# Kernel tuning notes

Hardware: AMD Instinct MI355X
Metric: run time of the kernel (lower is better)

Reference implementation:

```python
import jax, jax.numpy as jnp
import numpy as np

FS = 24000.0
C_SOUND = 343.0
MAX_TAU = 6
IGNORE = -100
PAIRS = np.array([(0, 1), (0, 2), (0, 3), (1, 2), (1, 3), (2, 3)])  # m1<m2 loop order
PERMS_NP = np.array([(0, 1, 2), (0, 2, 1), (1, 0, 2), (1, 2, 0), (2, 0, 1), (2, 1, 0)])  # itertools order


def _mic_locs():
    # [rad, azi_deg, ele_deg] per mic, centered at origin (matches center_mic_coords)
    coords = np.array([[0.042, 45, 35], [0.042, -45, -35], [0.042, 135, -35], [0.042, -135, 35]], dtype=np.float64)
    rad = coords[:, 0]
    azi = coords[:, 1] * 2 * np.pi / 360
    ele = coords[:, 2] * 2 * np.pi / 360
    locs = np.stack([rad * np.cos(azi) * np.cos(ele), rad * np.sin(azi) * np.cos(ele), rad * np.sin(ele)], axis=1)
    return jnp.asarray(locs, dtype=jnp.float32)

MIC_LOCS = _mic_locs()  # [4,3]


def _get_tdoa_targets(target):
    """Vectorized get_tdoa_target. target: [B,T,E,5,C].
    Assumes <=1 active class per (b,t,track) so the random class shuffle is a no-op.
    Returns (tdoas, tdoas2) as int32 [B,T,E,6]."""
    B, T, E, F, C = target.shape
    active = target[:, :, :, 0, :]                                  # [B,T,E,C] 0/1 flags
    is_active = jnp.any(active > 0, axis=-1)                        # [B,T,E]
    doa = jnp.einsum('btec,btedc->bted', active, target[:, :, :, 1:4, :])  # [B,T,E,3]
    dist = jnp.einsum('btec,btec->bte', active, target[:, :, :, 4, :])     # [B,T,E]
    src = doa * dist[..., None]                                     # [B,T,E,3]
    d = jnp.linalg.norm(src[..., None, :] - MIC_LOCS, axis=-1)      # [B,T,E,4] dist to each mic
    tdoa = d[..., PAIRS[:, 0]] - d[..., PAIRS[:, 1]]                # [B,T,E,6]
    tdoa = jnp.round(tdoa * FS / C_SOUND) + MAX_TAU                 # [B,T,E,6]
    # compact active tracks to the front (stable keeps track order, matching tr_cnt)
    order = jnp.argsort(jnp.logical_not(is_active), axis=-1)        # [B,T,E]
    gathered = jnp.take_along_axis(tdoa, order[..., None], axis=2)  # [B,T,E,6]
    n = jnp.sum(is_active, axis=-1)                                 # [B,T] number of events
    k = jnp.arange(E)[None, None, :]                                # slot index
    idx1 = jnp.clip(jnp.minimum(k, n[:, :, None] - 1), 0, E - 1)    # pad with LAST event
    idx2 = jnp.where(k < n[:, :, None], k, 0)                       # pad with FIRST event
    tdoas = jnp.take_along_axis(gathered, idx1[..., None], axis=2)
    tdoas2 = jnp.take_along_axis(gathered, idx2[..., None], axis=2)
    empty = (n == 0)[:, :, None, None]
    tdoas = jnp.where(empty, float(IGNORE), tdoas)
    tdoas2 = jnp.where(empty, float(IGNORE), tdoas2)
    return tdoas.astype(jnp.int32), tdoas2.astype(jnp.int32)


def _forward(pred, t_a, t_b):
    B, T, C, Tr, ntd = pred.shape
    N = B * T * ntd
    p = pred.transpose(0, 1, 4, 2, 3).reshape(N, C, Tr)             # [N,C,Tr]
    ta = t_a.transpose(0, 1, 3, 2).reshape(N, Tr)                   # [N,Tr]
    tb = t_b.transpose(0, 1, 3, 2).reshape(N, Tr)
    logp = jax.nn.log_softmax(p, axis=1)                            # [N,C,Tr]
    perms = jnp.asarray(PERMS_NP)                                   # [6,Tr]
    ar = jnp.arange(Tr)

    def pit(t):
        tc = jnp.clip(t, 0, C - 1)
        # L[n,i,j] = CE(pred track j, target track i); ignore_index -> 0
        L = -jnp.take_along_axis(logp, jnp.broadcast_to(tc[:, :, None], (N, Tr, Tr)), axis=1)
        L = jnp.where((t == IGNORE)[:, :, None], 0.0, L)
        pl = L[:, ar[None, :], perms].mean(axis=-1)                 # [N,6] per-perm mean loss
        pidx = jnp.argmin(pl, axis=1)                               # first min (matches torch loop)
        return jnp.take_along_axis(pl, pidx[:, None], axis=1)[:, 0], perms[pidx]

    loss1, perm1 = pit(ta)
    loss2, perm2 = pit(tb)
    use2 = loss2 < loss1                                            # torch.min keeps first on ties
    loss = jnp.where(use2, loss2, loss1)
    t_sel = jnp.where(use2[:, None], tb, ta)
    perm_sel = jnp.where(use2[:, None], perm2, perm1)

    pred_cls = jnp.argmax(p, axis=1)                                # [N,Tr]
    t_perm = jnp.take_along_axis(t_sel, perm_sel, axis=1)           # target reordered by opt perm
    valid = t_perm != IGNORE
    npred = jnp.sum(valid)
    correct = jnp.sum((pred_cls == t_perm) & valid)
    acc = jnp.where(npred > 0, correct.astype(jnp.float32) / jnp.maximum(npred, 1).astype(jnp.float32), 0.0)

    mask = loss > 0.0
    nval = jnp.sum(mask)
    lmean = jnp.where(nval > 0, jnp.sum(jnp.where(mask, loss, 0.0)) / jnp.maximum(nval, 1).astype(loss.dtype), 0.0)
    return lmean, acc


def setup_inputs() -> dict:
    key = jax.random.key(0)
    B, T, E, NCLS, NTD, CPRED = 128, 600, 3, 13, 6, 13
    k1, k2, k3, k4, k5 = jax.random.split(key, 5)
    pred = jax.random.normal(k1, (B, T, CPRED, E, NTD), dtype=jnp.float32)
    act_cls = jax.random.randint(k2, (B, T, E), 0, NCLS)
    act_flag = (jax.random.uniform(k3, (B, T, E)) < 0.5).astype(jnp.float32)
    onehot = jax.nn.one_hot(act_cls, NCLS, dtype=jnp.float32) * act_flag[..., None]  # <=1 active class/track
    doa = jax.random.normal(k4, (B, T, E, 3), dtype=jnp.float32)
    doa = doa / jnp.linalg.norm(doa, axis=-1, keepdims=True)
    dist = jax.random.uniform(k5, (B, T, E), minval=1.0, maxval=3.0, dtype=jnp.float32)
    target = jnp.concatenate([
        onehot[:, :, :, None, :],
        jnp.broadcast_to(doa[..., None], (B, T, E, 3, NCLS)),
        jnp.broadcast_to(dist[..., None, None], (B, T, E, 1, NCLS)),
    ], axis=3).astype(jnp.float32)                                  # [B,T,E,5,NCLS]
    return {"pred": pred, "target": target}


def reference(pred, target):
    t_a, t_b = _get_tdoa_targets(target)
    return _forward(pred, t_a, t_b)
```

## Files before the change

### kernel.cpp

```cpp
#include <hip/hip_runtime.h>
#include <cstdint>
#include <cstddef>

#define BT_TOTAL 76800
#define NCLS 13
#define IGN  (-100)

#define CPB   32
#define NTHR  192
#define NBLK  (BT_TOTAL / CPB)
#define NF4P  (CPB * 234 / 4)
#define KP    10
#define PADP  (KP * NTHR)

struct Partial { float ls; int lc; int cor; int val; };

__device__ __forceinline__ void stage16(const float4* g, float4* l) {
    __builtin_amdgcn_global_load_lds((const __attribute__((address_space(1))) void*)g,
                                     (__attribute__((address_space(3))) void*)l,
                                     16, 0, 0);
}

extern "C" __global__ __launch_bounds__(NTHR)
void tdoa_fused(const float* __restrict__ pred, const float* __restrict__ target,
                Partial* __restrict__ part) {
    const int tid = threadIdx.x;
    const int cb  = blockIdx.x * CPB;

    __shared__ float4 sP4[PADP];
    const float* sP = (const float*)sP4;

    {
        const float4* gp = (const float4*)(pred + (size_t)cb * 234);
#pragma unroll
        for (int r = 0; r < KP; r++) {
            const int i  = r * NTHR + tid;
            const int ic = (i < NF4P) ? i : (NF4P - 1);
            stage16(gp + ic, &sP4[i]);
        }
    }

    const int cell = tid / 6;
    const int p    = tid - cell * 6;
    const float* tg = target + (size_t)(cb + cell) * 195;

    const float MX[4] = { 0.02432757455f,  0.02432757455f, -0.02432757455f, -0.02432757455f };
    const float MY[4] = { 0.02432757455f, -0.02432757455f,  0.02432757455f, -0.02432757455f };
    const float MZ[4] = { 0.02409021033f, -0.02409021033f, -0.02409021033f,  0.02409021033f };
    const int PI_[6] = {0,0,0,1,1,2};
    const int PJ_[6] = {1,2,3,2,3,3};
    const int mi = PI_[p], mj = PJ_[p];
    const float mxi = MX[mi], myi = MY[mi], mzi = MZ[mi];
    const float mxj = MX[mj], myj = MY[mj], mzj = MZ[mj];

    int  td[3];
    bool ab[3];
    int  nact = 0;
#pragma unroll
    for (int e = 0; e < 3; e++) {
        float av = 0.f; int ci = 0; bool ia = false;
#pragma unroll
        for (int c = 0; c < NCLS; c++) {
            const float a = tg[e * 65 + c];
            const bool  g = (a > 0.0f);
            av = g ? a : av;
            ci = g ? c : ci;
            ia = ia || g;
        }
        const float d0 = av * tg[e * 65 + 13 + ci];
        const float d1 = av * tg[e * 65 + 26 + ci];
        const float d2 = av * tg[e * 65 + 39 + ci];
        const float ds = av * tg[e * 65 + 52 + ci];
        const float sx = d0 * ds, sy = d1 * ds, sz = d2 * ds;
        const float exi = sx - mxi, eyi = sy - myi, ezi = sz - mzi;
        const float exj = sx - mxj, eyj = sy - myj, ezj = sz - mzj;
        const float dmi = sqrtf(exi * exi + eyi * eyi + ezi * ezi);
        const float dmj = sqrtf(exj * exj + eyj * eyj + ezj * ezj);
        td[e] = (int)rintf((dmi - dmj) * (24000.0f / 343.0f)) + 6;
        ab[e] = ia;
        nact += ia ? 1 : 0;
    }

    const int g0 = ab[0] ? td[0] : (ab[1] ? td[1] : td[2]);
    const int g1 = (ab[0] && ab[1]) ? td[1] : td[2];
    const int g2 = td[2];
    int ta[3], tb[3];
    ta[0] = g0;
    ta[1] = (nact >= 2) ? g1 : g0;
    ta[2] = (nact == 3) ? g2 : ((nact == 2) ? g1 : g0);
    tb[0] = g0;
    tb[1] = (nact >= 2) ? g1 : g0;
    tb[2] = (nact == 3) ? g2 : g0;
    if (nact == 0) { ta[0] = ta[1] = ta[2] = IGN; tb[0] = tb[1] = tb[2] = IGN; }

    __syncthreads();

    const float* pp = sP + cell * 234 + p;

    float x[NCLS][3];
#pragma unroll
    for (int c = 0; c < NCLS; c++)
#pragma unroll
        for (int j = 0; j < 3; j++)
            x[c][j] = pp[c * 18 + j * 6];

    int   am[3];
    float lse[3];
#pragma unroll
    for (int j = 0; j < 3; j++) {
        float m = x[0][j]; int a = 0;
#pragma unroll
        for (int c = 1; c < NCLS; c++) { if (x[c][j] > m) { m = x[c][j]; a = c; } }
        float s = 0.f;
#pragma unroll
        for (int c = 0; c < NCLS; c++) s += expf(x[c][j] - m);
        am[j] = a; lse[j] = m + logf(s);
    }

    float La[3][3], Lb[3][3];
#pragma unroll
    for (int i = 0; i < 3; i++) {
        const int  ca  = (ta[i] < 0) ? 0 : ta[i];
        const int  cbb = (tb[i] < 0) ? 0 : tb[i];
        const bool ia2 = (ta[i] == IGN);
        const bool ib2 = (tb[i] == IGN);
#pragma unroll
        for (int j = 0; j < 3; j++) {
            La[i][j] = ia2 ? 0.f : (lse[j] - pp[ca  * 18 + j * 6]);
            Lb[i][j] = ib2 ? 0.f : (lse[j] - pp[cbb * 18 + j * 6]);
        }
    }

    const int P0[6] = {0,0,1,1,2,2};
    const int P1[6] = {1,2,0,2,0,1};
    const int P2[6] = {2,1,2,0,1,0};
    float l1 = 0.f, l2 = 0.f; int i1 = 0, i2 = 0;
#pragma unroll
    for (int q = 0; q < 6; q++) {
        const float va = (La[0][P0[q]] + La[1][P1[q]] + La[2][P2[q]]) * (1.0f / 3.0f);
        const float vb = (Lb[0][P0[q]] + Lb[1][P1[q]] + Lb[2][P2[q]]) * (1.0f / 3.0f);
        if (q == 0) { l1 = va; l2 = vb; }
        else {
            if (va < l1) { l1 = va; i1 = q; }
            if (vb < l2) { l2 = vb; i2 = q; }
        }
    }

    const bool use2 = (l2 < l1);
    const float loss = use2 ? l2 : l1;
    const int  qsel = use2 ? i2 : i1;
    const int PK[6] = {36, 24, 33, 9, 18, 6};
    int pk = PK[0];
#pragma unroll
    for (int k = 1; k < 6; k++) pk = (qsel == k) ? PK[k] : pk;
    const int s0 = use2 ? tb[0] : ta[0];
    const int s1 = use2 ? tb[1] : ta[1];
    const int s2 = use2 ? tb[2] : ta[2];

    float lsum = 0.f;
    int   lcnt = 0, cor = 0, nval = 0;
#pragma unroll
    for (int i = 0; i < 3; i++) {
        const int pi = (pk >> (2 * i)) & 3;
        const int tp = (pi == 0) ? s0 : ((pi == 1) ? s1 : s2);
        const bool v = (tp != IGN);
        nval += v ? 1 : 0;
        cor  += (v && (am[i] == tp)) ? 1 : 0;
    }
    if (loss > 0.f) { lsum += loss; lcnt++; }

#pragma unroll
    for (int off = 32; off > 0; off >>= 1) {
        lsum += __shfl_down(lsum, off, 64);
        lcnt += __shfl_down(lcnt, off, 64);
        cor  += __shfl_down(cor,  off, 64);
        nval += __shfl_down(nval, off, 64);
    }
    __shared__ float rf[3];
    __shared__ int   r1[3], r2[3], r3[3];
    const int wid = tid >> 6;
    if ((tid & 63) == 0) { rf[wid] = lsum; r1[wid] = lcnt; r2[wid] = cor; r3[wid] = nval; }
    __syncthreads();
    if (tid == 0) {
        Partial pt;
        pt.ls  = rf[0] + rf[1] + rf[2];
        pt.lc  = r1[0] + r1[1] + r1[2];
        pt.cor = r2[0] + r2[1] + r2[2];
        pt.val = r3[0] + r3[1] + r3[2];
        part[blockIdx.x] = pt;
    }
}

extern "C" __global__ __launch_bounds__(256)
void tdoa_final(const Partial* __restrict__ part, float* __restrict__ out) {
    const int tid = threadIdx.x;
    double ls = 0.0; int lc = 0, cor = 0, val = 0;
    for (int i = tid; i < NBLK; i += 256) {
        const Partial p = part[i];
        ls += (double)p.ls; lc += p.lc; cor += p.cor; val += p.val;
    }
#pragma unroll
    for (int off = 32; off > 0; off >>= 1) {
        ls  += __shfl_down(ls,  off, 64);
        lc  += __shfl_down(lc,  off, 64);
        cor += __shfl_down(cor, off, 64);
        val += __shfl_down(val, off, 64);
    }
    __shared__ double sd[4];
    __shared__ int    s1[4], s2[4], s3[4];
    const int wid = tid >> 6;
    if ((tid & 63) == 0) { sd[wid] = ls; s1[wid] = lc; s2[wid] = cor; s3[wid] = val; }
    __syncthreads();
    if (tid == 0) {
        const double L = sd[0] + sd[1] + sd[2] + sd[3];
        const int c1 = s1[0] + s1[1] + s1[2] + s1[3];
        const int c2 = s2[0] + s2[1] + s2[2] + s2[3];
        const int c3 = s3[0] + s3[1] + s3[2] + s3[3];
        out[0] = (c1 > 0) ? (float)(L / (double)c1) : 0.0f;
        out[1] = (c3 > 0) ? ((float)c2 / (float)c3) : 0.0f;
    }
}

extern "C" void kernel_launch(void* const* d_in, const int* in_sizes, int n_in,
                              void* d_out, int out_size, void* d_ws, size_t ws_size,
                              hipStream_t stream) {
    const float* pred   = (const float*)d_in[0];
    const float* target = (const float*)d_in[1];
    Partial* part = (Partial*)d_ws;
    float* out = (float*)d_out;
    hipLaunchKernelGGL(tdoa_fused, dim3(NBLK), dim3(NTHR), 0, stream, pred, target, part);
    hipLaunchKernelGGL(tdoa_final, dim3(1),    dim3(256), 0, stream, part, out);
}
```

Before: 156.0 us.

## Compute per-track TDOAs once per track in shared memory and use fast exp/log

Target processing is redistributed so that each pair of threads handles one (cell, track). They read the one-hot row and the doa/dist rows with a dot product, split across two half-threads. The unit computes all four mic distances once, packs six clamped TDOA values plus an active flag into a 32-bit word in shared memory, and the pair threads unpack them. This replaces the old scheme, where each of six pair threads per cell redundantly scanned all targets and did sqrt work. Softmax exp/log also switch to the fast intrinsics, trading a little accuracy. The TDOA values are newly clamped to 0..12, and a stray label sits in the loop.

```diff
diff --git a/kernel.cpp b/kernel.cpp
--- a/kernel.cpp
+++ b/kernel.cpp
@@ -27,7 +27,8 @@
     const int tid = threadIdx.x;
     const int cb  = blockIdx.x * CPB;
 
-    __shared__ float4 sP4[PADP];
+    __shared__ float4   sP4[PADP];
+    __shared__ uint32_t sTd[CPB * 3];
     const float* sP = (const float*)sP4;
 
     {
@@ -40,50 +41,77 @@
         }
     }
 
+    {
+        const int unit  = tid >> 1;
+        const int h     = tid & 1;
+        const int cellU = unit / 3;
+        const int e     = unit - cellU * 3;
+        const float* tgE = target + (size_t)(cb + cellU) * 195 + e * 65;
+
+        float d0 = 0.f, d1 = 0.f, d2 = 0.f, ds = 0.f;
+        bool  ia = false;
+#pragma unroll
+        for (int k = 0; k < 7; k++) {
+            if (h && k == 6) break;
+            const int c  = h ? (7 + k) : k;
+            const float a  = tgE[c];
+            const float r0 = tgE[13 + c];
+            const float r1 = tgE[26 + c];
+            const float r2 = tgE[39 + c];
+            const float r3 = tgE[52 + c];
+            ia = ia || (a > 0.0f);
+            d0 += a * r0;
+            d1 += a * r1;
+            d2 += a * r2;
+            d3_dummy:;
+            ds += a * r3;
+        }
+        d0 += __shfl_xor(d0, 1, 64);
+        d1 += __shfl_xor(d1, 1, 64);
+        d2 += __shfl_xor(d2, 1, 64);
+        ds += __shfl_xor(ds, 1, 64);
+        int iai = ia ? 1 : 0;
+        iai |= __shfl_xor(iai, 1, 64);
+
+        const float sx = d0 * ds, sy = d1 * ds, sz = d2 * ds;
+        const float MX[4] = { 0.02432757455f,  0.02432757455f, -0.02432757455f, -0.02432757455f };
+        const float MY[4] = { 0.02432757455f, -0.02432757455f,  0.02432757455f, -0.02432757455f };
+        const float MZ[4] = { 0.02409021033f, -0.02409021033f, -0.02409021033f,  0.02409021033f };
+        float dm[4];
+#pragma unroll
+        for (int m = 0; m < 4; m++) {
+            const float ex = sx - MX[m], ey = sy - MY[m], ez = sz - MZ[m];
+            dm[m] = sqrtf(ex * ex + ey * ey + ez * ez);
+        }
+        const int PI_[6] = {0,0,0,1,1,2};
+        const int PJ_[6] = {1,2,3,2,3,3};
+        uint32_t w = 0;
+#pragma unroll
+        for (int p = 0; p < 6; p++) {
+            int t = (int)rintf((dm[PI_[p]] - dm[PJ_[p]]) * (24000.0f / 343.0f)) + 6;
+            t = (t < 0) ? 0 : ((t > 12) ? 12 : t);
+            w |= ((uint32_t)t) << (4 * p);
+        }
+        if (iai) w |= (1u << 28);
+        if (h == 0) sTd[cellU * 3 + e] = w;
+    }
+
+    __syncthreads();
+
     const int cell = tid / 6;
     const int p    = tid - cell * 6;
-    const float* tg = target + (size_t)(cb + cell) * 195;
-
-    const float MX[4] = { 0.02432757455f,  0.02432757455f, -0.02432757455f, -0.02432757455f };
-    const float MY[4] = { 0.02432757455f, -0.02432757455f,  0.02432757455f, -0.02432757455f };
-    const float MZ[4] = { 0.02409021033f, -0.02409021033f, -0.02409021033f,  0.02409021033f };
-    const int PI_[6] = {0,0,0,1,1,2};
-    const int PJ_[6] = {1,2,3,2,3,3};
-    const int mi = PI_[p], mj = PJ_[p];
-    const float mxi = MX[mi], myi = MY[mi], mzi = MZ[mi];
-    const float mxj = MX[mj], myj = MY[mj], mzj = MZ[mj];
-
-    int  td[3];
-    bool ab[3];
-    int  nact = 0;
-#pragma unroll
-    for (int e = 0; e < 3; e++) {
-        float av = 0.f; int ci = 0; bool ia = false;
-#pragma unroll
-        for (int c = 0; c < NCLS; c++) {
-            const float a = tg[e * 65 + c];
-            const bool  g = (a > 0.0f);
-            av = g ? a : av;
-            ci = g ? c : ci;
-            ia = ia || g;
-        }
-        const float d0 = av * tg[e * 65 + 13 + ci];
-        const float d1 = av * tg[e * 65 + 26 + ci];
-        const float d2 = av * tg[e * 65 + 39 + ci];
-        const float ds = av * tg[e * 65 + 52 + ci];
-        const float sx = d0 * ds, sy = d1 * ds, sz = d2 * ds;
-        const float exi = sx - mxi, eyi = sy - myi, ezi = sz - mzi;
-        const float exj = sx - mxj, eyj = sy - myj, ezj = sz - mzj;
-        const float dmi = sqrtf(exi * exi + eyi * eyi + ezi * ezi);
-        const float dmj = sqrtf(exj * exj + eyj * eyj + ezj * ezj);
-        td[e] = (int)rintf((dmi - dmj) * (24000.0f / 343.0f)) + 6;
-        ab[e] = ia;
-        nact += ia ? 1 : 0;
-    }
-
-    const int g0 = ab[0] ? td[0] : (ab[1] ? td[1] : td[2]);
-    const int g1 = (ab[0] && ab[1]) ? td[1] : td[2];
-    const int g2 = td[2];
+
+    const uint32_t t0 = sTd[cell * 3 + 0];
+    const uint32_t t1 = sTd[cell * 3 + 1];
+    const uint32_t t2 = sTd[cell * 3 + 2];
+    const bool ab0 = (t0 >> 28) & 1, ab1 = (t1 >> 28) & 1, ab2 = (t2 >> 28) & 1;
+    const int  nact = (int)ab0 + (int)ab1 + (int)ab2;
+    const int  v0 = (int)((t0 >> (4 * p)) & 15);
+    const int  v1 = (int)((t1 >> (4 * p)) & 15);
+    const int  v2 = (int)((t2 >> (4 * p)) & 15);
+    const int  g0 = ab0 ? v0 : (ab1 ? v1 : v2);
+    const int  g1 = (ab0 && ab1) ? v1 : v2;
+    const int  g2 = v2;
     int ta[3], tb[3];
     ta[0] = g0;
     ta[1] = (nact >= 2) ? g1 : g0;
@@ -93,8 +121,6 @@
     tb[2] = (nact == 3) ? g2 : g0;
     if (nact == 0) { ta[0] = ta[1] = ta[2] = IGN; tb[0] = tb[1] = tb[2] = IGN; }
 
-    __syncthreads();
-
     const float* pp = sP + cell * 234 + p;
 
     float x[NCLS][3];
@@ -113,8 +139,8 @@
         for (int c = 1; c < NCLS; c++) { if (x[c][j] > m) { m = x[c][j]; a = c; } }
         float s = 0.f;
 #pragma unroll
-        for (int c = 0; c < NCLS; c++) s += expf(x[c][j] - m);
-        am[j] = a; lse[j] = m + logf(s);
+        for (int c = 0; c < NCLS; c++) s += __expf(x[c][j] - m);
+        am[j] = a; lse[j] = m + __logf(s);
     }
 
     float La[3][3], Lb[3][3];
```

New measurement: 156.3 us. Within noise of the previous version (+0.2%).
